# Kernel tuning notes

Measured on AMD Instinct MI355X. Metric: run time of the kernel, lower is better.

The kernel has to match this reference:

```python
import jax, jax.numpy as jnp
import numpy as np
from jax import lax

# Conv config (mirrors Conv2dMem init_kwargs)
B, CIN, H, W = 16, 256, 56, 56
COUT, K = 256, 3
STRIDE, PAD = 1, 1
INPUT_BW = 8   # sum(input_slice [1,1,2,4])
WEIGHT_BW = 8  # sum(weight_slice [1,1,2,4])
IN_GRAN = (1, 32)    # input_quant_gran
W_GRAN = (32, 32)    # weight_quant_gran
H_OUT = (H + 2 * PAD - K) // STRIDE + 1
W_OUT = (W + 2 * PAD - K) // STRIDE + 1


def block_fake_quant(x, gran, bw):
    """Per-block symmetric fake quantization to `bw` bits (1 sign bit).

    Blocks of size gran=(gr, gc) over the last two dims share one max-abs scale.
    Bit-slicing then exactly recombines to this quantized integer, so the
    ideal (noise-free) MapReduceDot math equals this quant-dequant + GEMM.
    """
    gr, gc = gran
    lead = x.shape[:-2]
    R, C = x.shape[-2], x.shape[-1]
    xb = x.reshape(*lead, R // gr, gr, C // gc, gc)
    m = jnp.max(jnp.abs(xb), axis=(-3, -1), keepdims=True)
    levels = 2.0 ** (bw - 1) - 1.0
    scale = jnp.where(m > 0, m / levels, jnp.ones_like(m))
    xq = jnp.round(xb / scale) * scale
    return xq.reshape(x.shape)


def setup_inputs() -> dict:
    key = jax.random.key(0)
    kx, kw, kb = jax.random.split(key, 3)
    x = jax.random.normal(kx, (B, CIN, H, W), dtype=jnp.float32)
    fan_in = CIN * K * K
    # kaiming_uniform(a=sqrt(5)) -> U(-1/sqrt(fan_in), 1/sqrt(fan_in))
    bound = 1.0 / np.sqrt(fan_in)
    weight = jax.random.uniform(kw, (COUT, CIN, K, K), dtype=jnp.float32,
                                minval=-bound, maxval=bound)
    bias = jax.random.uniform(kb, (COUT,), dtype=jnp.float32,
                              minval=-bound, maxval=bound)
    return {"x": x, "weight": weight, "bias": bias}


def reference(x, weight, bias):
    # Unfold: (B, CIN*K*K, H_OUT*W_OUT) with torch-compatible (c, kh, kw) feature order
    patches = lax.conv_general_dilated_patches(
        x, filter_shape=(K, K), window_strides=(STRIDE, STRIDE),
        padding=((PAD, PAD), (PAD, PAD)))
    L = H_OUT * W_OUT
    cdim = CIN * K * K
    inp_unf = patches.reshape(B, cdim, L).transpose(0, 2, 1)  # (B, L, cdim)
    # Per-block quantize input (gran (1,32) over (L, cdim)) and weight (gran (32,32))
    xq = block_fake_quant(inp_unf, IN_GRAN, INPUT_BW)
    wmat = weight.reshape(COUT, cdim).T  # (cdim, COUT)
    wq = block_fake_quant(wmat, W_GRAN, WEIGHT_BW)
    out = jnp.einsum('blc,co->blo', xq, wq) + bias  # (B, L, COUT)
    # fold with 1x1 kernel == reshape back to image layout
    return out.transpose(0, 2, 1).reshape(B, COUT, H_OUT, W_OUT)
```

## Files before the change

kernel.cpp:

```cpp
#include <hip/hip_runtime.h>

typedef unsigned short u16;
typedef unsigned int u32;
typedef __bf16 bf16x8 __attribute__((ext_vector_type(8)));
typedef float f32x4 __attribute__((ext_vector_type(4)));
typedef u32 u32x4 __attribute__((ext_vector_type(4)));

#define CIN 256
#define COUT_ 256
#define HW 56
#define LIMG 3136
#define CDIM 2304
#define NSTEP 36
#define NTILE 392

static __device__ __forceinline__ u16 f32_bf16(float f) {
    u32 u = __float_as_uint(f);
    u += 0x7fffu + ((u >> 16) & 1u);
    return (u16)(u >> 16);
}

__global__ void quant_w_kernel(const float* __restrict__ w, u16* __restrict__ wq) {
    const int kb = blockIdx.x % 72;
    const int ob = blockIdx.x / 72;
    const int k0 = kb * 32, o0 = ob * 32;
    const int t = threadIdx.x;
    float v[16];
    float mx = 0.f;
#pragma unroll
    for (int i = 0; i < 16; ++i) {
        const int e = i * 64 + t;
        const int oo = e >> 5, cc = e & 31;
        const float val = w[(o0 + oo) * CDIM + k0 + cc];
        v[i] = val;
        mx = fmaxf(mx, fabsf(val));
    }
#pragma unroll
    for (int d = 1; d < 64; d <<= 1) mx = fmaxf(mx, __shfl_xor(mx, d, 64));
    const float scale = mx > 0.f ? mx * (1.f / 127.f) : 1.f;
    const float inv   = mx > 0.f ? 127.f / mx : 1.f;
#pragma unroll
    for (int i = 0; i < 16; ++i) {
        const int e = i * 64 + t;
        const int oo = e >> 5, cc = e & 31;
        const int o = o0 + oo, k = k0 + cc;
        const float q = rintf(v[i] * inv) * scale;
        wq[o * CDIM + (k ^ ((o & 7) << 3))] = f32_bf16(q);
    }
}

__global__ __launch_bounds__(256, 2)
void conv_gemm_kernel(const float* __restrict__ x, const u16* __restrict__ wq,
                      const float* __restrict__ bias, float* __restrict__ out) {
    __shared__ __align__(16) u16 Bs[256 * 64];
    __shared__ __align__(16) u16 As[128 * 64];

    const int tid  = threadIdx.x;
    const int lane = tid & 63;
    const int wid  = __builtin_amdgcn_readfirstlane(tid >> 6);
    const int wm   = wid & 1;
    const int wn   = wid >> 1;
    const int h    = wn;

    const int tile = (blockIdx.x & 7) * 49 + (blockIdx.x >> 3);
    const int m0   = tile * 128;

    const int r = wm * 64 + lane;
    const int m = m0 + r;
    const int img = m / 3136;
    const int l   = m - img * 3136;
    const int oh  = l / HW, ow = l - (l / HW) * HW;

    u32 pb = 0;
#pragma unroll
    for (int p = 0; p < 9; ++p) {
        const int kh = p / 3, kw = p - (p / 3) * 3;
        const int ih = oh + kh - 1, iw = ow + kw - 1;
        const u32 ok = (ih >= 0 && ih < HW && iw >= 0 && iw < HW) ? 1u : 0u;
        pb |= ok << p;
    }
    const float* __restrict__ xim = x + (size_t)img * (CIN * LIMG);

    f32x4 acc[4][8];
#pragma unroll
    for (int mi = 0; mi < 4; ++mi)
#pragma unroll
        for (int n = 0; n < 8; ++n)
            acc[mi][n] = (f32x4){0.f, 0.f, 0.f, 0.f};

    float va[32];

    auto gather_issue = [&](int t) {
#pragma unroll
        for (int j = 0; j < 32; ++j) {
            const int k = t * 64 + h * 32 + j;
            const int c = k / 9;
            const int p = k - c * 9;
            const int kh = p / 3;
            const int dsp = (kh - 1) * HW + (p - kh * 3) - 1;
            int e = l + dsp;
            e = min(max(e, 0), LIMG - 1);
            va[j] = xim[(u32)(c * LIMG + e)];
        }
    };

    gather_issue(0);

#pragma unroll 1
    for (int t = 0; t < NSTEP; ++t) {
#pragma unroll
        for (int i = 0; i < 8; ++i) {
            const int colt = i * 32 + (tid >> 3);
            const u16* g = wq + (size_t)colt * CDIM + t * 64 + (tid & 7) * 8;
            u16* lp = &Bs[0] + i * 2048 + tid * 8;
            __builtin_amdgcn_global_load_lds(
                (const __attribute__((address_space(1))) void*)g,
                (__attribute__((address_space(3))) void*)lp, 16, 0, 0);
        }
        asm volatile("" ::: "memory");
        __builtin_amdgcn_sched_barrier(0);

#pragma unroll
        for (int j = 0; j < 32; ++j) {
            const int k = t * 64 + h * 32 + j;
            const int c = k / 9;
            const int p = k - c * 9;
            const u32 bit = (pb >> p) & 1u;
            va[j] = __uint_as_float(__float_as_uint(va[j]) & (0u - bit));
        }
        float t16[16];
#pragma unroll
        for (int j = 0; j < 16; ++j) t16[j] = fmaxf(fabsf(va[j]), fabsf(va[j + 16]));
#pragma unroll
        for (int j = 0; j < 8; ++j) t16[j] = fmaxf(t16[j], t16[j + 8]);
#pragma unroll
        for (int j = 0; j < 4; ++j) t16[j] = fmaxf(t16[j], t16[j + 4]);
        const float mx = fmaxf(fmaxf(t16[0], t16[1]), fmaxf(t16[2], t16[3]));

        const float inv   = mx > 0.f ? 127.f * __builtin_amdgcn_rcpf(mx) : 0.f;
        const float scale = mx * (1.f / 127.f);

        union { u16 hh[32]; u32x4 v4[4]; } pk;
#pragma unroll
        for (int j = 0; j < 32; ++j)
            pk.hh[j] = f32_bf16(rintf(va[j] * inv) * scale);
#pragma unroll
        for (int w = 0; w < 4; ++w) {
            const int s = h * 4 + w;
            *(u32x4*)&As[r * 64 + ((s ^ (r & 7)) << 3)] = pk.v4[w];
        }
        asm volatile("" ::: "memory");
        __builtin_amdgcn_sched_barrier(0);

        if (t < NSTEP - 1) {
            gather_issue(t + 1);
            asm volatile("s_waitcnt lgkmcnt(0) vmcnt(32)" ::: "memory");
        } else {
            asm volatile("s_waitcnt lgkmcnt(0) vmcnt(0)" ::: "memory");
        }
        __builtin_amdgcn_sched_barrier(0);
        __builtin_amdgcn_s_barrier();
        asm volatile("" ::: "memory");
        __builtin_amdgcn_sched_barrier(0);

        const int arow_b = wm * 64 + (lane & 15);
        const int bcol_b = wn * 128 + (lane & 15);
        const int sl = lane >> 4;
#pragma unroll
        for (int kk = 0; kk < 2; ++kk) {
            const int s = kk * 4 + sl;
            bf16x8 a[4];
#pragma unroll
            for (int mi = 0; mi < 4; ++mi) {
                const int ar = arow_b + mi * 16;
                a[mi] = *(const bf16x8*)&As[ar * 64 + ((s ^ (ar & 7)) << 3)];
            }
#pragma unroll
            for (int n = 0; n < 8; ++n) {
                const int col = bcol_b + n * 16;
                const bf16x8 b = *(const bf16x8*)&Bs[col * 64 + ((s ^ (col & 7)) << 3)];
#pragma unroll
                for (int mi = 0; mi < 4; ++mi)
                    acc[mi][n] = __builtin_amdgcn_mfma_f32_16x16x32_bf16(a[mi], b, acc[mi][n], 0, 0, 0);
            }
        }
        asm volatile("" ::: "memory");
        __builtin_amdgcn_sched_barrier(0);
        __builtin_amdgcn_s_barrier();
        asm volatile("" ::: "memory");
        __builtin_amdgcn_sched_barrier(0);
    }

    const int si    = __builtin_amdgcn_readfirstlane(m0 / 3136);
    const int l0    = m0 - si * 3136;
    const bool split = l0 > 3136 - 128;
    const int rb = wm * 64 + ((lane >> 4) << 2);
#pragma unroll
    for (int n = 0; n < 8; ++n) {
        const int col = wn * 128 + n * 16 + (lane & 15);
        const float bz = bias[col];
#pragma unroll
        for (int mi = 0; mi < 4; ++mi) {
            f32x4 a = acc[mi][n];
            a[0] += bz; a[1] += bz; a[2] += bz; a[3] += bz;
            const int row = rb + mi * 16;
            if (!split) {
                *(f32x4*)&out[((size_t)(si * COUT_ + col)) * LIMG + l0 + row] = a;
            } else {
#pragma unroll
                for (int j = 0; j < 4; ++j) {
                    const int mm = m0 + row + j;
                    const int ig = mm / 3136;
                    const int ll = mm - ig * 3136;
                    out[((size_t)(ig * COUT_ + col)) * LIMG + ll] = a[j];
                }
            }
        }
    }
}

extern "C" void kernel_launch(void* const* d_in, const int* in_sizes, int n_in,
                              void* d_out, int out_size, void* d_ws, size_t ws_size,
                              hipStream_t stream) {
    const float* x    = (const float*)d_in[0];
    const float* w    = (const float*)d_in[1];
    const float* bias = (const float*)d_in[2];
    float* out = (float*)d_out;
    u16* wq = (u16*)d_ws;

    quant_w_kernel<<<576, 64, 0, stream>>>(w, wq);
    conv_gemm_kernel<<<NTILE, 256, 0, stream>>>(x, wq, bias, out);
}
```

Before: 259.7 us.

## Split output channels across two blocks and precompute gather offsets

Halves the per-block N tile to 128 columns and doubles the grid, so each block holds fewer accumulators and less LDS and can run at higher occupancy. Gather addresses and padding masks are precomputed once per thread and rotated each step instead of recomputed with divisions. It also raises MFMA wave priority and uses the native bf16 conversion. The cost is that each input patch tile is gathered and quantized twice, once per N half.

```diff
diff --git a/kernel.cpp b/kernel.cpp
--- a/kernel.cpp
+++ b/kernel.cpp
@@ -10,15 +10,10 @@
 #define COUT_ 256
 #define HW 56
 #define LIMG 3136
+#define XIMG (CIN * LIMG)
 #define CDIM 2304
 #define NSTEP 36
-#define NTILE 392
-
-static __device__ __forceinline__ u16 f32_bf16(float f) {
-    u32 u = __float_as_uint(f);
-    u += 0x7fffu + ((u >> 16) & 1u);
-    return (u16)(u >> 16);
-}
+#define GRID 784
 
 __global__ void quant_w_kernel(const float* __restrict__ w, u16* __restrict__ wq) {
     const int kb = blockIdx.x % 72;
@@ -45,14 +40,15 @@
         const int oo = e >> 5, cc = e & 31;
         const int o = o0 + oo, k = k0 + cc;
         const float q = rintf(v[i] * inv) * scale;
-        wq[o * CDIM + (k ^ ((o & 7) << 3))] = f32_bf16(q);
+        const u32 b = __float_as_uint(q) + 0x7fffu + ((__float_as_uint(q) >> 16) & 1u);
+        wq[o * CDIM + (k ^ ((o & 7) << 3))] = (u16)(b >> 16);
     }
 }
 
-__global__ __launch_bounds__(256, 2)
+__global__ __launch_bounds__(256, 3)
 void conv_gemm_kernel(const float* __restrict__ x, const u16* __restrict__ wq,
                       const float* __restrict__ bias, float* __restrict__ out) {
-    __shared__ __align__(16) u16 Bs[256 * 64];
+    __shared__ __align__(16) u16 Bs[128 * 64];
     __shared__ __align__(16) u16 As[128 * 64];
 
     const int tid  = threadIdx.x;
@@ -62,8 +58,9 @@
     const int wn   = wid >> 1;
     const int h    = wn;
 
-    const int tile = (blockIdx.x & 7) * 49 + (blockIdx.x >> 3);
-    const int m0   = tile * 128;
+    const int bid = (blockIdx.x & 7) * 98 + (blockIdx.x >> 3);
+    const int mt = bid >> 1, nt = bid & 1;
+    const int m0 = mt * 128, n0 = nt * 128;
 
     const int r = wm * 64 + lane;
     const int m = m0 + r;
@@ -79,29 +76,39 @@
         const u32 ok = (ih >= 0 && ih < HW && iw >= 0 && iw < HW) ? 1u : 0u;
         pb |= ok << p;
     }
-    const float* __restrict__ xim = x + (size_t)img * (CIN * LIMG);
-
-    f32x4 acc[4][8];
+
+    u32 roff[9], rmb[9];
+#pragma unroll
+    for (int q = 0; q < 9; ++q) {
+        const int p = (h * 32 + q) % 9;
+        const int kh = p / 3;
+        const int dsp = (kh - 1) * HW + (p - kh * 3) - 1;
+        int e = l + dsp;
+        e = min(max(e, 0), LIMG - 1);
+        roff[q] = (u32)(img * XIMG + e) * 4u;
+        rmb[q]  = 0u - ((pb >> p) & 1u);
+    }
+
+    f32x4 acc[4][4];
 #pragma unroll
     for (int mi = 0; mi < 4; ++mi)
 #pragma unroll
-        for (int n = 0; n < 8; ++n)
+        for (int n = 0; n < 4; ++n)
             acc[mi][n] = (f32x4){0.f, 0.f, 0.f, 0.f};
 
     float va[32];
 
     auto gather_issue = [&](int t) {
+        const int k0 = t * 64 + h * 32;
 #pragma unroll
         for (int j = 0; j < 32; ++j) {
-            const int k = t * 64 + h * 32 + j;
-            const int c = k / 9;
-            const int p = k - c * 9;
-            const int kh = p / 3;
-            const int dsp = (kh - 1) * HW + (p - kh * 3) - 1;
-            int e = l + dsp;
-            e = min(max(e, 0), LIMG - 1);
-            va[j] = xim[(u32)(c * LIMG + e)];
-        }
+            const u32 soff = (u32)(((k0 + j) / 9) * (LIMG * 4));
+            va[j] = *(const float*)((const char*)x + (roff[j % 9] + soff));
+        }
+        u32 t0 = roff[0];
+#pragma unroll
+        for (int q = 0; q < 8; ++q) roff[q] = roff[q + 1];
+        roff[8] = t0;
     };
 
     gather_issue(0);
@@ -109,8 +116,8 @@
 #pragma unroll 1
     for (int t = 0; t < NSTEP; ++t) {
 #pragma unroll
-        for (int i = 0; i < 8; ++i) {
-            const int colt = i * 32 + (tid >> 3);
+        for (int i = 0; i < 4; ++i) {
+            const int colt = n0 + i * 32 + (tid >> 3);
             const u16* g = wq + (size_t)colt * CDIM + t * 64 + (tid & 7) * 8;
             u16* lp = &Bs[0] + i * 2048 + tid * 8;
             __builtin_amdgcn_global_load_lds(
@@ -121,29 +128,32 @@
         __builtin_amdgcn_sched_barrier(0);
 
 #pragma unroll
-        for (int j = 0; j < 32; ++j) {
-            const int k = t * 64 + h * 32 + j;
-            const int c = k / 9;
-            const int p = k - c * 9;
-            const u32 bit = (pb >> p) & 1u;
-            va[j] = __uint_as_float(__float_as_uint(va[j]) & (0u - bit));
+        for (int j = 0; j < 32; ++j)
+            va[j] = __uint_as_float(__float_as_uint(va[j]) & rmb[j % 9]);
+        {
+            u32 t0 = rmb[0];
+#pragma unroll
+            for (int q = 0; q < 8; ++q) rmb[q] = rmb[q + 1];
+            rmb[8] = t0;
         }
         float t16[16];
 #pragma unroll
         for (int j = 0; j < 16; ++j) t16[j] = fmaxf(fabsf(va[j]), fabsf(va[j + 16]));
-#pragma unroll
-        for (int j = 0; j < 8; ++j) t16[j] = fmaxf(t16[j], t16[j + 8]);
-#pragma unroll
-        for (int j = 0; j < 4; ++j) t16[j] = fmaxf(t16[j], t16[j + 4]);
-        const float mx = fmaxf(fmaxf(t16[0], t16[1]), fmaxf(t16[2], t16[3]));
+        float m8[8];
+#pragma unroll
+        for (int j = 0; j < 8; ++j) m8[j] = fmaxf(t16[j], t16[j + 8]);
+        const float ma = fmaxf(fmaxf(m8[0], m8[1]), m8[2]);
+        const float mb = fmaxf(fmaxf(m8[3], m8[4]), m8[5]);
+        const float mc = fmaxf(m8[6], m8[7]);
+        const float mx = fmaxf(fmaxf(ma, mb), mc);
 
         const float inv   = mx > 0.f ? 127.f * __builtin_amdgcn_rcpf(mx) : 0.f;
         const float scale = mx * (1.f / 127.f);
 
-        union { u16 hh[32]; u32x4 v4[4]; } pk;
+        union { __bf16 hh[32]; u32x4 v4[4]; } pk;
 #pragma unroll
         for (int j = 0; j < 32; ++j)
-            pk.hh[j] = f32_bf16(rintf(va[j] * inv) * scale);
+            pk.hh[j] = (__bf16)(rintf(va[j] * inv) * scale);
 #pragma unroll
         for (int w = 0; w < 4; ++w) {
             const int s = h * 4 + w;
@@ -164,26 +174,30 @@
         __builtin_amdgcn_sched_barrier(0);
 
         const int arow_b = wm * 64 + (lane & 15);
-        const int bcol_b = wn * 128 + (lane & 15);
+        const int bcol_b = wn * 64 + (lane & 15);
         const int sl = lane >> 4;
+        __builtin_amdgcn_s_setprio(1);
 #pragma unroll
         for (int kk = 0; kk < 2; ++kk) {
             const int s = kk * 4 + sl;
-            bf16x8 a[4];
+            bf16x8 a[4], b[4];
 #pragma unroll
             for (int mi = 0; mi < 4; ++mi) {
                 const int ar = arow_b + mi * 16;
                 a[mi] = *(const bf16x8*)&As[ar * 64 + ((s ^ (ar & 7)) << 3)];
             }
 #pragma unroll
-            for (int n = 0; n < 8; ++n) {
-                const int col = bcol_b + n * 16;
-                const bf16x8 b = *(const bf16x8*)&Bs[col * 64 + ((s ^ (col & 7)) << 3)];
+            for (int n = 0; n < 4; ++n) {
+                const int cl = bcol_b + n * 16;
+                b[n] = *(const bf16x8*)&Bs[cl * 64 + ((s ^ (cl & 7)) << 3)];
+            }
+#pragma unroll
+            for (int n = 0; n < 4; ++n)
 #pragma unroll
                 for (int mi = 0; mi < 4; ++mi)
-                    acc[mi][n] = __builtin_amdgcn_mfma_f32_16x16x32_bf16(a[mi], b, acc[mi][n], 0, 0, 0);
-            }
-        }
+                    acc[mi][n] = __builtin_amdgcn_mfma_f32_16x16x32_bf16(a[mi], b[n], acc[mi][n], 0, 0, 0);
+        }
+        __builtin_amdgcn_s_setprio(0);
         asm volatile("" ::: "memory");
         __builtin_amdgcn_sched_barrier(0);
         __builtin_amdgcn_s_barrier();
@@ -196,8 +210,8 @@
     const bool split = l0 > 3136 - 128;
     const int rb = wm * 64 + ((lane >> 4) << 2);
 #pragma unroll
-    for (int n = 0; n < 8; ++n) {
-        const int col = wn * 128 + n * 16 + (lane & 15);
+    for (int n = 0; n < 4; ++n) {
+        const int col = n0 + wn * 64 + n * 16 + (lane & 15);
         const float bz = bias[col];
 #pragma unroll
         for (int mi = 0; mi < 4; ++mi) {
@@ -229,5 +243,5 @@
     u16* wq = (u16*)d_ws;
 
     quant_w_kernel<<<576, 64, 0, stream>>>(w, wq);
-    conv_gemm_kernel<<<NTILE, 256, 0, stream>>>(x, wq, bias, out);
+    conv_gemm_kernel<<<GRID, 256, 0, stream>>>(x, wq, bias, out);
 }
```

After: 262.5 us. No clear change (+1.1%).
